# Kernel optimization log

Hardware: AMD Instinct MI355X
Metric: run time of the kernel (lower is better)

Reference implementation:

```python
import jax, jax.numpy as jnp
import numpy as np

BETA = 0.1       # reputation weight
GAMMA = 0.1      # load penalty weight
EXPL_C = 0.1     # UCB exploration constant
LOAD_EMA = 0.9   # load EMA alpha
TOP_K = 2
EPS = 1e-10


def setup_inputs() -> dict:
    key = jax.random.key(0)
    k1, k2, k3, k4, k5 = jax.random.split(key, 5)
    B, S, H, E = 4, 4096, 2048, 64
    return {
        "x": jax.random.normal(k1, (B, S, H), dtype=jnp.float32),
        "gate_w": jax.random.normal(k2, (E, H), dtype=jnp.float32) * (1.0 / np.sqrt(H)),
        "reputation": jax.random.normal(k3, (E,), dtype=jnp.float32),
        "loads": jax.random.uniform(k4, (E,), dtype=jnp.float32),
        "counts": jax.random.uniform(k5, (E,), dtype=jnp.float32),
        "total_decisions": 1000000,
    }


def reference(x, gate_w, reputation, loads, counts, total_decisions):
    B, S, H = x.shape
    E = gate_w.shape[0]
    x_flat = x.reshape(-1, H)                                  # [T, H]
    base_logits = jnp.einsum("th,eh->te", x_flat, gate_w)      # [T, E]

    # current_batch_assignments is None -> current_loads = expert_loads
    updated_loads = LOAD_EMA * loads + (1.0 - LOAD_EMA) * loads  # [E]

    # UCB-style exploration bonus, broadcast over tokens
    expl = EXPL_C * jnp.sqrt(jnp.log(jnp.float32(total_decisions) + 1.0) / (counts + EPS))  # [E]

    selection_scores = (base_logits
                        + BETA * reputation[None, :]
                        - GAMMA * updated_loads[None, :]
                        + expl[None, :])                        # [T, E]

    top_k_scores, top_k_indices = jax.lax.top_k(selection_scores, TOP_K)  # [T, K]
    routing_weights = jax.nn.softmax(top_k_scores, axis=-1).reshape(B, S, TOP_K)
    expert_indices = top_k_indices.reshape(B, S, TOP_K)

    # differentiable load-balancing aux loss
    router_probs = jax.nn.softmax(selection_scores.astype(jnp.float32), axis=-1)  # [T, E]
    expert_gate = jax.nn.one_hot(top_k_indices, E, dtype=jnp.float32).sum(axis=1)  # [T, E]
    tokens_per_expert = expert_gate.mean(axis=0)               # [E]
    router_prob_per_expert = router_probs.mean(axis=0)         # [E]
    aux_loss = (tokens_per_expert * router_prob_per_expert).sum() * E

    return routing_weights, expert_indices, aux_loss
```

## Files before the change

### kernel.cpp

```cpp
#include <hip/hip_runtime.h>
#include <cmath>

#define HDIM 2048
#define H4   (HDIM / 4)
#define NEXP 64
#define TTOT 16384
#define KSPLIT 2
#define KBLK (HDIM / KSPLIT)
#define BKC  64
#define NCHUNK (KBLK / BKC)
#define BTOK 64
#define LDT  72
#define LDS_SC 65

#define WS_PARTIAL_OFF 128
#define PARTIAL_FLOATS ((size_t)(TTOT / BTOK) * KSPLIT * BTOK * NEXP)

typedef short  bf16x8 __attribute__((ext_vector_type(8)));
typedef float  f32x4  __attribute__((ext_vector_type(4)));

__device__ __forceinline__ short f2bf_rn(float f, float* back) {
    unsigned u = __float_as_uint(f);
    unsigned r = (u + 0x7fffu + ((u >> 16) & 1u)) & 0xffff0000u;
    *back = __uint_as_float(r);
    return (short)(r >> 16);
}

__global__ __launch_bounds__(256, 2) void router_gemm_mfma(
    const float* __restrict__ x,
    const float* __restrict__ gw,
    float* __restrict__ partial)
{
    __shared__ short aT[3][BTOK][LDT];
    __shared__ short bT[3][NEXP][LDT];

    const int tid  = threadIdx.x;
    const int lane = tid & 63;
    const int quad = lane >> 4;
    const int l15  = lane & 15;
    const int w    = tid >> 6;
    const int wm   = w & 1;
    const int wn   = w >> 1;
    const int tb   = blockIdx.x;
    const int kg   = blockIdx.y;
    const int T0   = tb * BTOK;

    const int srow = tid >> 2;
    const int scol = tid & 3;

    const float4* __restrict__ x4 = reinterpret_cast<const float4*>(x);
    const float4* __restrict__ g4 = reinterpret_cast<const float4*>(gw);

    f32x4 acc[2][2];
    #pragma unroll
    for (int i = 0; i < 2; ++i)
        #pragma unroll
        for (int j = 0; j < 2; ++j)
            acc[i][j] = (f32x4){0.f, 0.f, 0.f, 0.f};

    float4 xa[4], xb[4];

#define LOAD_CHUNK(CH) do {                                                    \
        const int _c4b = kg * (H4 / 2) + (CH) * (BKC / 4);                     \
        _Pragma("unroll")                                                      \
        for (int j = 0; j < 4; ++j) {                                          \
            xa[j] = x4[(size_t)(T0 + srow) * H4 + _c4b + scol + 4 * j];        \
            xb[j] = g4[(size_t)srow * H4 + _c4b + scol + 4 * j];               \
        } } while (0)

#define SPLIT_STORE(TILE, ROW, KLOC, FV) do {                                  \
        const float _f[4] = {(FV).x, (FV).y, (FV).z, (FV).w};                  \
        short _h[4], _m[4], _l[4];                                             \
        _Pragma("unroll")                                                      \
        for (int u = 0; u < 4; ++u) {                                          \
            float _b0, _b1, _b2;                                               \
            _h[u] = f2bf_rn(_f[u], &_b0);                                      \
            float _r1 = _f[u] - _b0;                                           \
            _m[u] = f2bf_rn(_r1, &_b1);                                        \
            float _r2 = _r1 - _b1;                                             \
            _l[u] = f2bf_rn(_r2, &_b2);                                        \
        }                                                                      \
        *reinterpret_cast<short4*>(&TILE[0][ROW][KLOC]) =                      \
            make_short4(_h[0], _h[1], _h[2], _h[3]);                           \
        *reinterpret_cast<short4*>(&TILE[1][ROW][KLOC]) =                      \
            make_short4(_m[0], _m[1], _m[2], _m[3]);                           \
        *reinterpret_cast<short4*>(&TILE[2][ROW][KLOC]) =                      \
            make_short4(_l[0], _l[1], _l[2], _l[3]);                           \
    } while (0)

    LOAD_CHUNK(0);

    for (int ch = 0; ch < NCHUNK; ++ch) {
        #pragma unroll
        for (int j = 0; j < 4; ++j) {
            const int kloc = 4 * (scol + 4 * j);
            SPLIT_STORE(aT, srow, kloc, xa[j]);
            SPLIT_STORE(bT, srow, kloc, xb[j]);
        }
        __syncthreads();

        if (ch + 1 < NCHUNK) LOAD_CHUNK(ch + 1);

        #pragma unroll
        for (int k0 = 0; k0 < BKC; k0 += 32) {
            const int kf = k0 + quad * 8;
            bf16x8 ah[2], am[2], al[2], bh[2], bm[2], bl[2];
            #pragma unroll
            for (int mt = 0; mt < 2; ++mt) {
                const int row = 32 * wm + 16 * mt + l15;
                ah[mt] = *reinterpret_cast<const bf16x8*>(&aT[0][row][kf]);
                am[mt] = *reinterpret_cast<const bf16x8*>(&aT[1][row][kf]);
                al[mt] = *reinterpret_cast<const bf16x8*>(&aT[2][row][kf]);
            }
            #pragma unroll
            for (int nt = 0; nt < 2; ++nt) {
                const int row = 32 * wn + 16 * nt + l15;
                bh[nt] = *reinterpret_cast<const bf16x8*>(&bT[0][row][kf]);
                bm[nt] = *reinterpret_cast<const bf16x8*>(&bT[1][row][kf]);
                bl[nt] = *reinterpret_cast<const bf16x8*>(&bT[2][row][kf]);
            }
            #pragma unroll
            for (int mt = 0; mt < 2; ++mt)
                #pragma unroll
                for (int nt = 0; nt < 2; ++nt) {
                    f32x4 c = acc[mt][nt];
                    c = __builtin_amdgcn_mfma_f32_16x16x32_bf16(ah[mt], bh[nt], c, 0, 0, 0);
                    c = __builtin_amdgcn_mfma_f32_16x16x32_bf16(ah[mt], bm[nt], c, 0, 0, 0);
                    c = __builtin_amdgcn_mfma_f32_16x16x32_bf16(am[mt], bh[nt], c, 0, 0, 0);
                    c = __builtin_amdgcn_mfma_f32_16x16x32_bf16(ah[mt], bl[nt], c, 0, 0, 0);
                    c = __builtin_amdgcn_mfma_f32_16x16x32_bf16(am[mt], bm[nt], c, 0, 0, 0);
                    c = __builtin_amdgcn_mfma_f32_16x16x32_bf16(al[mt], bh[nt], c, 0, 0, 0);
                    acc[mt][nt] = c;
                }
        }
        __syncthreads();
    }
#undef LOAD_CHUNK
#undef SPLIT_STORE

    float* pbase = partial + ((size_t)tb * KSPLIT + kg) * (BTOK * NEXP);
    #pragma unroll
    for (int mt = 0; mt < 2; ++mt)
        #pragma unroll
        for (int nt = 0; nt < 2; ++nt) {
            const int e = 32 * wn + 16 * nt + l15;
            #pragma unroll
            for (int r = 0; r < 4; ++r) {
                const int t_loc = 32 * wm + 16 * mt + quad * 4 + r;
                pbase[(size_t)t_loc * NEXP + e] = acc[mt][nt][r];
            }
        }
}

__global__ __launch_bounds__(256) void router_reduce(
    const float* __restrict__ partial,
    const float* __restrict__ rep,
    const float* __restrict__ loads,
    const float* __restrict__ counts,
    const int*   __restrict__ total_dec,
    float* __restrict__ out_w,
    float* __restrict__ out_idx,
    float* __restrict__ prob_acc,
    float* __restrict__ gate_acc)
{
    __shared__ float sc_s[BTOK][LDS_SC];
    __shared__ float bias_s[NEXP];
    __shared__ float m_s[BTOK], z_s[BTOK];
    __shared__ int   i1_s[BTOK], i2_s[BTOK];

    const int tid = threadIdx.x;
    const int rt  = blockIdx.x;
    const int t0  = rt * BTOK;

    if (tid < NEXP) {
        float L = logf((float)(*total_dec) + 1.0f);
        bias_s[tid] = 0.1f * rep[tid] - 0.1f * loads[tid]
                    + 0.1f * sqrtf(L / (counts[tid] + 1e-10f));
    }
    __syncthreads();

    const float* p = partial + (size_t)rt * KSPLIT * (BTOK * NEXP);
    #pragma unroll
    for (int o = 0; o < (BTOK * NEXP) / 256; ++o) {
        const int idx = o * 256 + tid;
        float s = p[idx] + p[BTOK * NEXP + idx];
        sc_s[idx >> 6][idx & 63] = s + bias_s[idx & 63];
    }
    __syncthreads();

    if (tid < BTOK) {
        const int t = tid;
        float m1 = -INFINITY, m2 = -INFINITY;
        int   i1 = 0, i2 = 0;
        for (int e = 0; e < NEXP; ++e) {
            const float s = sc_s[t][e];
            if (s > m1)      { m2 = m1; i2 = i1; m1 = s; i1 = e; }
            else if (s > m2) { m2 = s; i2 = e; }
        }
        float z = 0.0f;
        for (int e = 0; e < NEXP; ++e) z += expf(sc_s[t][e] - m1);

        const float e2  = expf(m2 - m1);
        const float inv = 1.0f / (1.0f + e2);
        const int   gt  = t0 + t;
        reinterpret_cast<float2*>(out_w)[gt]   = make_float2(inv, e2 * inv);
        reinterpret_cast<float2*>(out_idx)[gt] = make_float2((float)i1, (float)i2);
        m_s[t] = m1; z_s[t] = z; i1_s[t] = i1; i2_s[t] = i2;
    }
    __syncthreads();

    if (tid < NEXP) {
        const int e = tid;
        float ps = 0.0f, gs = 0.0f;
        for (int t = 0; t < BTOK; ++t) {
            ps += expf(sc_s[t][e] - m_s[t]) / z_s[t];
            gs += (float)((i1_s[t] == e) + (i2_s[t] == e));
        }
        atomicAdd(&prob_acc[e], ps);
        atomicAdd(&gate_acc[e], gs);
    }
}

#define BKF  32
#define LDAF (64 + 4)
__global__ __launch_bounds__(256) void router_main(
    const float* __restrict__ x,
    const float* __restrict__ gw,
    const float* __restrict__ rep,
    const float* __restrict__ loads,
    const float* __restrict__ counts,
    const int*   __restrict__ total_dec,
    float* __restrict__ out_w,
    float* __restrict__ out_idx,
    float* __restrict__ prob_acc,
    float* __restrict__ gate_acc)
{
    __shared__ float a_s[2][BKF][LDAF];
    __shared__ float b_s[2][BKF][LDAF];
    __shared__ float sc_s[64][LDS_SC];
    __shared__ float bias_s[NEXP];
    __shared__ float m_s[64], z_s[64];
    __shared__ int   i1_s[64], i2_s[64];

    const int tid = threadIdx.x;
    const int tx  = tid & 15;
    const int ty  = tid >> 4;
    const int r0  = tid >> 3;
    const int c4  = tid & 7;
    const int t0  = blockIdx.x * 64;

    if (tid < NEXP) {
        float L = logf((float)(*total_dec) + 1.0f);
        bias_s[tid] = 0.1f * rep[tid] - 0.1f * loads[tid]
                    + 0.1f * sqrtf(L / (counts[tid] + 1e-10f));
    }

    const float4* __restrict__ x4 = reinterpret_cast<const float4*>(x) + (size_t)t0 * H4;
    const float4* __restrict__ g4 = reinterpret_cast<const float4*>(gw);

    float acc[4][4] = {};

#define STORE_TILE(BUFI, A0, A1, B0, B1) do {                                  \
        float _t0[4] = {(A0).x, (A0).y, (A0).z, (A0).w};                       \
        float _t1[4] = {(A1).x, (A1).y, (A1).z, (A1).w};                       \
        float _t2[4] = {(B0).x, (B0).y, (B0).z, (B0).w};                       \
        float _t3[4] = {(B1).x, (B1).y, (B1).z, (B1).w};                       \
        _Pragma("unroll")                                                      \
        for (int u = 0; u < 4; ++u) {                                          \
            a_s[BUFI][c4 * 4 + u][r0]      = _t0[u];                           \
            a_s[BUFI][c4 * 4 + u][r0 + 32] = _t1[u];                           \
            b_s[BUFI][c4 * 4 + u][r0]      = _t2[u];                           \
            b_s[BUFI][c4 * 4 + u][r0 + 32] = _t3[u];                           \
        } } while (0)

    {
        float4 a0 = x4[(size_t)r0 * H4 + c4];
        float4 a1 = x4[(size_t)(r0 + 32) * H4 + c4];
        float4 b0 = g4[(size_t)r0 * H4 + c4];
        float4 b1 = g4[(size_t)(r0 + 32) * H4 + c4];
        STORE_TILE(0, a0, a1, b0, b1);
    }
    __syncthreads();

    int buf = 0;
    for (int it = 0; it < HDIM / BKF; ++it) {
        float4 na0, na1, nb0, nb1;
        const bool has_next = (it + 1 < HDIM / BKF);
        if (has_next) {
            const int k4 = (it + 1) * (BKF / 4);
            na0 = x4[(size_t)r0 * H4 + k4 + c4];
            na1 = x4[(size_t)(r0 + 32) * H4 + k4 + c4];
            nb0 = g4[(size_t)r0 * H4 + k4 + c4];
            nb1 = g4[(size_t)(r0 + 32) * H4 + k4 + c4];
        }
        #pragma unroll
        for (int kk = 0; kk < BKF; ++kk) {
            const float4 afv = *reinterpret_cast<const float4*>(&a_s[buf][kk][ty * 4]);
            const float4 bfv = *reinterpret_cast<const float4*>(&b_s[buf][kk][tx * 4]);
            const float af[4] = {afv.x, afv.y, afv.z, afv.w};
            const float bf[4] = {bfv.x, bfv.y, bfv.z, bfv.w};
            #pragma unroll
            for (int i = 0; i < 4; ++i)
                #pragma unroll
                for (int j = 0; j < 4; ++j)
                    acc[i][j] = fmaf(af[i], bf[j], acc[i][j]);
        }
        if (has_next) STORE_TILE(buf ^ 1, na0, na1, nb0, nb1);
        __syncthreads();
        buf ^= 1;
    }
#undef STORE_TILE

    #pragma unroll
    for (int i = 0; i < 4; ++i)
        #pragma unroll
        for (int j = 0; j < 4; ++j)
            sc_s[ty * 4 + i][tx * 4 + j] = acc[i][j] + bias_s[tx * 4 + j];
    __syncthreads();

    if (tid < 64) {
        const int t = tid;
        float m1 = -INFINITY, m2 = -INFINITY;
        int   i1 = 0, i2 = 0;
        for (int e = 0; e < NEXP; ++e) {
            const float s = sc_s[t][e];
            if (s > m1)      { m2 = m1; i2 = i1; m1 = s; i1 = e; }
            else if (s > m2) { m2 = s; i2 = e; }
        }
        float z = 0.0f;
        for (int e = 0; e < NEXP; ++e) z += expf(sc_s[t][e] - m1);
        const float e2  = expf(m2 - m1);
        const float inv = 1.0f / (1.0f + e2);
        const int   gt  = t0 + t;
        reinterpret_cast<float2*>(out_w)[gt]   = make_float2(inv, e2 * inv);
        reinterpret_cast<float2*>(out_idx)[gt] = make_float2((float)i1, (float)i2);
        m_s[t] = m1; z_s[t] = z; i1_s[t] = i1; i2_s[t] = i2;
    }
    __syncthreads();

    if (tid < NEXP) {
        const int e = tid;
        float ps = 0.0f, gs = 0.0f;
        for (int t = 0; t < 64; ++t) {
            ps += expf(sc_s[t][e] - m_s[t]) / z_s[t];
            gs += (float)((i1_s[t] == e) + (i2_s[t] == e));
        }
        atomicAdd(&prob_acc[e], ps);
        atomicAdd(&gate_acc[e], gs);
    }
}

__global__ void router_aux(const float* __restrict__ prob_acc,
                           const float* __restrict__ gate_acc,
                           float* __restrict__ out_aux)
{
    const float invT = 1.0f / (float)TTOT;
    const int e = threadIdx.x;
    float v = (gate_acc[e] * invT) * (prob_acc[e] * invT);
    #pragma unroll
    for (int off = 32; off > 0; off >>= 1)
        v += __shfl_down(v, off);
    if (e == 0) out_aux[0] = v * (float)NEXP;
}

extern "C" void kernel_launch(void* const* d_in, const int* in_sizes, int n_in,
                              void* d_out, int out_size, void* d_ws, size_t ws_size,
                              hipStream_t stream)
{
    const float* x      = (const float*)d_in[0];
    const float* gw     = (const float*)d_in[1];
    const float* rep    = (const float*)d_in[2];
    const float* loads  = (const float*)d_in[3];
    const float* counts = (const float*)d_in[4];
    const int*   total  = (const int*)d_in[5];

    float* out     = (float*)d_out;
    float* out_w   = out;
    float* out_idx = out + 32768;
    float* out_aux = out + 65536;

    float* prob_acc = (float*)d_ws;
    float* gate_acc = prob_acc + NEXP;
    float* partial  = (float*)d_ws + WS_PARTIAL_OFF;

    const size_t ws_needed = (WS_PARTIAL_OFF + PARTIAL_FLOATS) * sizeof(float);

    hipMemsetAsync(d_ws, 0, WS_PARTIAL_OFF * sizeof(float), stream);

    if (ws_size >= ws_needed) {
        router_gemm_mfma<<<dim3(TTOT / BTOK, KSPLIT), dim3(256), 0, stream>>>(x, gw, partial);
        router_reduce<<<dim3(TTOT / BTOK), dim3(256), 0, stream>>>(
            partial, rep, loads, counts, total, out_w, out_idx, prob_acc, gate_acc);
    } else {
        router_main<<<dim3(TTOT / 64), dim3(256), 0, stream>>>(
            x, gw, rep, loads, counts, total, out_w, out_idx, prob_acc, gate_acc);
    }
    router_aux<<<dim3(1), dim3(64), 0, stream>>>(prob_acc, gate_acc, out_aux);
}
```

Measured before the change: 235.2 us.

## Use 32x32x16 MFMA, cheaper bf16 split, fused accumulator zeroing, fast exp

Replaces the four 16x16x32 MFMA tiles per wave with a single 32x32x16 MFMA tile, which cuts LDS fragment reads and simplifies the epilogue. The three-way bf16 split now truncates the low term with a cheap rounding add and packs pairs with perm instead of building shorts. The separate memset of the aux accumulators is removed and the GEMM kernel zeroes them instead, saving one launch. The reduce kernel uses __expf and multiplies by a precomputed reciprocal. Zeroing inside the GEMM relies on it finishing before the reduce kernel's atomics, which holds because both run in order on one stream.

Result: faster. 228.9 us (-2.7%).

```diff
diff --git a/kernel.cpp b/kernel.cpp
--- a/kernel.cpp
+++ b/kernel.cpp
@@ -17,27 +17,28 @@
 #define PARTIAL_FLOATS ((size_t)(TTOT / BTOK) * KSPLIT * BTOK * NEXP)
 
 typedef short  bf16x8 __attribute__((ext_vector_type(8)));
-typedef float  f32x4  __attribute__((ext_vector_type(4)));
-
-__device__ __forceinline__ short f2bf_rn(float f, float* back) {
+typedef float  f32x16 __attribute__((ext_vector_type(16)));
+
+__device__ __forceinline__ unsigned bf_rn_u(float f, float* back) {
     unsigned u = __float_as_uint(f);
     unsigned r = (u + 0x7fffu + ((u >> 16) & 1u)) & 0xffff0000u;
     *back = __uint_as_float(r);
-    return (short)(r >> 16);
+    return r;
 }
 
 __global__ __launch_bounds__(256, 2) void router_gemm_mfma(
     const float* __restrict__ x,
     const float* __restrict__ gw,
-    float* __restrict__ partial)
+    float* __restrict__ partial,
+    float* __restrict__ accs)
 {
     __shared__ short aT[3][BTOK][LDT];
     __shared__ short bT[3][NEXP][LDT];
 
     const int tid  = threadIdx.x;
     const int lane = tid & 63;
-    const int quad = lane >> 4;
-    const int l15  = lane & 15;
+    const int l31  = lane & 31;
+    const int lhi  = lane >> 5;
     const int w    = tid >> 6;
     const int wm   = w & 1;
     const int wn   = w >> 1;
@@ -45,47 +46,59 @@
     const int kg   = blockIdx.y;
     const int T0   = tb * BTOK;
 
+    if (tb == 0 && kg == 0 && tid < 2 * NEXP) accs[tid] = 0.0f;
+
     const int srow = tid >> 2;
     const int scol = tid & 3;
 
-    const float4* __restrict__ x4 = reinterpret_cast<const float4*>(x);
-    const float4* __restrict__ g4 = reinterpret_cast<const float4*>(gw);
-
-    f32x4 acc[2][2];
-    #pragma unroll
-    for (int i = 0; i < 2; ++i)
-        #pragma unroll
-        for (int j = 0; j < 2; ++j)
-            acc[i][j] = (f32x4){0.f, 0.f, 0.f, 0.f};
+    const float4* __restrict__ x4 = reinterpret_cast<const float4*>(x)
+        + (size_t)(T0 + srow) * H4 + (size_t)kg * (H4 / 2) + scol;
+    const float4* __restrict__ g4 = reinterpret_cast<const float4*>(gw)
+        + (size_t)srow * H4 + (size_t)kg * (H4 / 2) + scol;
+
+    f32x16 acc;
+    #pragma unroll
+    for (int i = 0; i < 16; ++i) acc[i] = 0.0f;
+
+    const short* aP[3];
+    const short* bP[3];
+    #pragma unroll
+    for (int v = 0; v < 3; ++v) {
+        aP[v] = &aT[v][32 * wm + l31][8 * lhi];
+        bP[v] = &bT[v][32 * wn + l31][8 * lhi];
+    }
 
     float4 xa[4], xb[4];
 
 #define LOAD_CHUNK(CH) do {                                                    \
-        const int _c4b = kg * (H4 / 2) + (CH) * (BKC / 4);                     \
         _Pragma("unroll")                                                      \
         for (int j = 0; j < 4; ++j) {                                          \
-            xa[j] = x4[(size_t)(T0 + srow) * H4 + _c4b + scol + 4 * j];        \
-            xb[j] = g4[(size_t)srow * H4 + _c4b + scol + 4 * j];               \
+            xa[j] = x4[(CH) * (BKC / 4) + 4 * j];                              \
+            xb[j] = g4[(CH) * (BKC / 4) + 4 * j];                              \
         } } while (0)
 
-#define SPLIT_STORE(TILE, ROW, KLOC, FV) do {                                  \
+#define SPLIT_STORE(TILE, ROW, FV, JJ) do {                                    \
         const float _f[4] = {(FV).x, (FV).y, (FV).z, (FV).w};                  \
-        short _h[4], _m[4], _l[4];                                             \
+        unsigned _h[4], _m[4], _l[4];                                          \
         _Pragma("unroll")                                                      \
         for (int u = 0; u < 4; ++u) {                                          \
-            float _b0, _b1, _b2;                                               \
-            _h[u] = f2bf_rn(_f[u], &_b0);                                      \
-            float _r1 = _f[u] - _b0;                                           \
-            _m[u] = f2bf_rn(_r1, &_b1);                                        \
-            float _r2 = _r1 - _b1;                                             \
-            _l[u] = f2bf_rn(_r2, &_b2);                                        \
+            float _b0, _b1;                                                    \
+            _h[u] = bf_rn_u(_f[u], &_b0);                                      \
+            const float _r1 = _f[u] - _b0;                                     \
+            _m[u] = bf_rn_u(_r1, &_b1);                                        \
+            const float _r2 = _r1 - _b1;                                       \
+            _l[u] = __float_as_uint(_r2) + 0x8000u;                            \
         }                                                                      \
-        *reinterpret_cast<short4*>(&TILE[0][ROW][KLOC]) =                      \
-            make_short4(_h[0], _h[1], _h[2], _h[3]);                           \
-        *reinterpret_cast<short4*>(&TILE[1][ROW][KLOC]) =                      \
-            make_short4(_m[0], _m[1], _m[2], _m[3]);                           \
-        *reinterpret_cast<short4*>(&TILE[2][ROW][KLOC]) =                      \
-            make_short4(_l[0], _l[1], _l[2], _l[3]);                           \
+        const int _kl = 4 * (scol + 4 * (JJ));                                 \
+        *reinterpret_cast<uint2*>(&TILE[0][ROW][_kl]) =                        \
+            make_uint2(__builtin_amdgcn_perm(_h[1], _h[0], 0x07060302u),       \
+                       __builtin_amdgcn_perm(_h[3], _h[2], 0x07060302u));      \
+        *reinterpret_cast<uint2*>(&TILE[1][ROW][_kl]) =                        \
+            make_uint2(__builtin_amdgcn_perm(_m[1], _m[0], 0x07060302u),       \
+                       __builtin_amdgcn_perm(_m[3], _m[2], 0x07060302u));      \
+        *reinterpret_cast<uint2*>(&TILE[2][ROW][_kl]) =                        \
+            make_uint2(__builtin_amdgcn_perm(_l[1], _l[0], 0x07060302u),       \
+                       __builtin_amdgcn_perm(_l[3], _l[2], 0x07060302u));      \
     } while (0)
 
     LOAD_CHUNK(0);
@@ -93,45 +106,27 @@
     for (int ch = 0; ch < NCHUNK; ++ch) {
         #pragma unroll
         for (int j = 0; j < 4; ++j) {
-            const int kloc = 4 * (scol + 4 * j);
-            SPLIT_STORE(aT, srow, kloc, xa[j]);
-            SPLIT_STORE(bT, srow, kloc, xb[j]);
+            SPLIT_STORE(aT, srow, xa[j], j);
+            SPLIT_STORE(bT, srow, xb[j], j);
         }
         __syncthreads();
 
         if (ch + 1 < NCHUNK) LOAD_CHUNK(ch + 1);
 
         #pragma unroll
-        for (int k0 = 0; k0 < BKC; k0 += 32) {
-            const int kf = k0 + quad * 8;
-            bf16x8 ah[2], am[2], al[2], bh[2], bm[2], bl[2];
-            #pragma unroll
-            for (int mt = 0; mt < 2; ++mt) {
-                const int row = 32 * wm + 16 * mt + l15;
-                ah[mt] = *reinterpret_cast<const bf16x8*>(&aT[0][row][kf]);
-                am[mt] = *reinterpret_cast<const bf16x8*>(&aT[1][row][kf]);
-                al[mt] = *reinterpret_cast<const bf16x8*>(&aT[2][row][kf]);
-            }
-            #pragma unroll
-            for (int nt = 0; nt < 2; ++nt) {
-                const int row = 32 * wn + 16 * nt + l15;
-                bh[nt] = *reinterpret_cast<const bf16x8*>(&bT[0][row][kf]);
-                bm[nt] = *reinterpret_cast<const bf16x8*>(&bT[1][row][kf]);
-                bl[nt] = *reinterpret_cast<const bf16x8*>(&bT[2][row][kf]);
-            }
-            #pragma unroll
-            for (int mt = 0; mt < 2; ++mt)
-                #pragma unroll
-                for (int nt = 0; nt < 2; ++nt) {
-                    f32x4 c = acc[mt][nt];
-                    c = __builtin_amdgcn_mfma_f32_16x16x32_bf16(ah[mt], bh[nt], c, 0, 0, 0);
-                    c = __builtin_amdgcn_mfma_f32_16x16x32_bf16(ah[mt], bm[nt], c, 0, 0, 0);
-                    c = __builtin_amdgcn_mfma_f32_16x16x32_bf16(am[mt], bh[nt], c, 0, 0, 0);
-                    c = __builtin_amdgcn_mfma_f32_16x16x32_bf16(ah[mt], bl[nt], c, 0, 0, 0);
-                    c = __builtin_amdgcn_mfma_f32_16x16x32_bf16(am[mt], bm[nt], c, 0, 0, 0);
-                    c = __builtin_amdgcn_mfma_f32_16x16x32_bf16(al[mt], bh[nt], c, 0, 0, 0);
-                    acc[mt][nt] = c;
-                }
+        for (int ks = 0; ks < 4; ++ks) {
+            bf16x8 ah = *reinterpret_cast<const bf16x8*>(aP[0] + 16 * ks);
+            bf16x8 am = *reinterpret_cast<const bf16x8*>(aP[1] + 16 * ks);
+            bf16x8 al = *reinterpret_cast<const bf16x8*>(aP[2] + 16 * ks);
+            bf16x8 bh = *reinterpret_cast<const bf16x8*>(bP[0] + 16 * ks);
+            bf16x8 bm = *reinterpret_cast<const bf16x8*>(bP[1] + 16 * ks);
+            bf16x8 bl = *reinterpret_cast<const bf16x8*>(bP[2] + 16 * ks);
+            acc = __builtin_amdgcn_mfma_f32_32x32x16_bf16(ah, bh, acc, 0, 0, 0);
+            acc = __builtin_amdgcn_mfma_f32_32x32x16_bf16(ah, bm, acc, 0, 0, 0);
+            acc = __builtin_amdgcn_mfma_f32_32x32x16_bf16(am, bh, acc, 0, 0, 0);
+            acc = __builtin_amdgcn_mfma_f32_32x32x16_bf16(ah, bl, acc, 0, 0, 0);
+            acc = __builtin_amdgcn_mfma_f32_32x32x16_bf16(am, bm, acc, 0, 0, 0);
+            acc = __builtin_amdgcn_mfma_f32_32x32x16_bf16(al, bh, acc, 0, 0, 0);
         }
         __syncthreads();
     }
@@ -139,17 +134,12 @@
 #undef SPLIT_STORE
 
     float* pbase = partial + ((size_t)tb * KSPLIT + kg) * (BTOK * NEXP);
-    #pragma unroll
-    for (int mt = 0; mt < 2; ++mt)
-        #pragma unroll
-        for (int nt = 0; nt < 2; ++nt) {
-            const int e = 32 * wn + 16 * nt + l15;
-            #pragma unroll
-            for (int r = 0; r < 4; ++r) {
-                const int t_loc = 32 * wm + 16 * mt + quad * 4 + r;
-                pbase[(size_t)t_loc * NEXP + e] = acc[mt][nt][r];
-            }
-        }
+    const int e = 32 * wn + l31;
+    #pragma unroll
+    for (int r = 0; r < 16; ++r) {
+        const int t_loc = 32 * wm + (r & 3) + 8 * (r >> 2) + 4 * lhi;
+        pbase[(size_t)t_loc * NEXP + e] = acc[r];
+    }
 }
 
 __global__ __launch_bounds__(256) void router_reduce(
@@ -165,7 +155,7 @@
 {
     __shared__ float sc_s[BTOK][LDS_SC];
     __shared__ float bias_s[NEXP];
-    __shared__ float m_s[BTOK], z_s[BTOK];
+    __shared__ float m_s[BTOK], zi_s[BTOK];
     __shared__ int   i1_s[BTOK], i2_s[BTOK];
 
     const int tid = threadIdx.x;
@@ -198,14 +188,14 @@
             else if (s > m2) { m2 = s; i2 = e; }
         }
         float z = 0.0f;
-        for (int e = 0; e < NEXP; ++e) z += expf(sc_s[t][e] - m1);
+        for (int e = 0; e < NEXP; ++e) z += __expf(sc_s[t][e] - m1);
 
         const float e2  = expf(m2 - m1);
         const float inv = 1.0f / (1.0f + e2);
         const int   gt  = t0 + t;
         reinterpret_cast<float2*>(out_w)[gt]   = make_float2(inv, e2 * inv);
         reinterpret_cast<float2*>(out_idx)[gt] = make_float2((float)i1, (float)i2);
-        m_s[t] = m1; z_s[t] = z; i1_s[t] = i1; i2_s[t] = i2;
+        m_s[t] = m1; zi_s[t] = 1.0f / z; i1_s[t] = i1; i2_s[t] = i2;
     }
     __syncthreads();
 
@@ -213,7 +203,7 @@
         const int e = tid;
         float ps = 0.0f, gs = 0.0f;
         for (int t = 0; t < BTOK; ++t) {
-            ps += expf(sc_s[t][e] - m_s[t]) / z_s[t];
+            ps += __expf(sc_s[t][e] - m_s[t]) * zi_s[t];
             gs += (float)((i1_s[t] == e) + (i2_s[t] == e));
         }
         atomicAdd(&prob_acc[e], ps);
@@ -385,13 +375,13 @@
 
     const size_t ws_needed = (WS_PARTIAL_OFF + PARTIAL_FLOATS) * sizeof(float);
 
-    hipMemsetAsync(d_ws, 0, WS_PARTIAL_OFF * sizeof(float), stream);
-
     if (ws_size >= ws_needed) {
-        router_gemm_mfma<<<dim3(TTOT / BTOK, KSPLIT), dim3(256), 0, stream>>>(x, gw, partial);
+        router_gemm_mfma<<<dim3(TTOT / BTOK, KSPLIT), dim3(256), 0, stream>>>(
+            x, gw, partial, prob_acc);
         router_reduce<<<dim3(TTOT / BTOK), dim3(256), 0, stream>>>(
             partial, rep, loads, counts, total, out_w, out_idx, prob_acc, gate_acc);
     } else {
+        hipMemsetAsync(d_ws, 0, WS_PARTIAL_OFF * sizeof(float), stream);
         router_main<<<dim3(TTOT / 64), dim3(256), 0, stream>>>(
             x, gw, rep, loads, counts, total, out_w, out_idx, prob_acc, gate_acc);
     }
```
